# Optimization experiments

Measured on AMD Instinct MI355X. Metric: run time of the kernel, lower is better.

Reference implementation:

```python
import jax, jax.numpy as jnp
import numpy as np

N = 50000          # nodes
E = 800000         # edges (avg degree 16)
C = 64             # hidden_channels
MC = 128           # message_channels = 2*C
EDGE_IN = 3 * C + 4
UPD_IN = C + MC + C


def _mlp(x, w1, b1, w2, b2, w3, b3):
    h1 = jax.nn.gelu(x @ w1 + b1, approximate=False)  # torch nn.GELU default = exact erf
    h2 = jax.nn.gelu(h1 @ w2 + b2, approximate=False)
    return h2 @ w3 + b3


def _layernorm(x, g, b, eps=1e-5):
    mu = x.mean(-1, keepdims=True)
    var = ((x - mu) ** 2).mean(-1, keepdims=True)
    return (x - mu) * jax.lax.rsqrt(var + eps) * g + b


def _forward(edge_index, coords, h, flow_dir, ln_g, ln_b,
             ew1, eb1, ew2, eb2, ew3, eb3,
             gw1, gb1, gw2, gb2,
             glw1, glb1, glw2, glb2, glw3, glb3,
             uw1, ub1, uw2, ub2, uw3, ub3, res_scale):
    x = coords[0]                       # [N,3]
    feat = _layernorm(h[0], ln_g, ln_b) # [N,C]
    u = flow_dir[0]
    u = u / (jnp.linalg.norm(u) + 1e-8)
    row, col = edge_index[0], edge_index[1]
    xi, xj = x[row], x[col]             # [E,3] gathers
    rel = xi - xj
    dist2 = (rel * rel).sum(-1, keepdims=True)
    xi_dot_u = (xi * u).sum(-1, keepdims=True)
    xj_dot_u = (xj * u).sum(-1, keepdims=True)
    rel_dot_u = (rel * u).sum(-1, keepdims=True)
    fi, fj = feat[row], feat[col]       # [E,C]
    fd = fi - fj
    edge_input = jnp.concatenate([fi, fj, fd, dist2, xi_dot_u, xj_dot_u, rel_dot_u], axis=-1)  # [E, 3C+4]
    edge_hidden = _mlp(edge_input, ew1, eb1, ew2, eb2, ew3, eb3)  # [E, MC]
    gate = jax.nn.sigmoid(jax.nn.gelu(edge_hidden @ gw1 + gb1, approximate=False) @ gw2 + gb2)  # [E,1]
    msg = gate * edge_hidden
    agg = jax.ops.segment_sum(msg, row, num_segments=N)                       # [N, MC]
    deg = jax.ops.segment_sum(jnp.ones((E, 1), feat.dtype), row, num_segments=N)
    agg = agg / jnp.maximum(deg, 1.0)
    global_feat = feat.mean(0, keepdims=True)                                  # [1,C]
    global_ctx = _mlp(global_feat, glw1, glb1, glw2, glb2, glw3, glb3)        # [1,C]
    global_node = jnp.broadcast_to(global_ctx, (feat.shape[0], global_ctx.shape[-1]))
    update_input = jnp.concatenate([feat, agg, global_node], axis=-1)          # [N, C+MC+C]
    dh = _mlp(update_input, uw1, ub1, uw2, ub2, uw3, ub3)                      # [N,C]
    return (jnp.tanh(res_scale) * dh)[None]                                    # [1,N,C]


def setup_inputs() -> dict:
    key = jax.random.key(0)
    ks = iter(jax.random.split(key, 40))
    def nrm(shape, scale=0.05):
        return (jax.random.normal(next(ks), shape, jnp.float32) * scale)
    return {
        "coords": jax.random.normal(next(ks), (1, N, 3), jnp.float32),
        "h": jax.random.normal(next(ks), (1, N, C), jnp.float32),
        "flow_dir": jax.random.normal(next(ks), (1, 3), jnp.float32),
        "edge_index": jax.random.randint(next(ks), (2, E), 0, N, dtype=jnp.int32),
        "ln_g": jnp.ones((C,), jnp.float32), "ln_b": jnp.zeros((C,), jnp.float32),
        "ew1": nrm((EDGE_IN, MC)), "eb1": jnp.zeros((MC,), jnp.float32),
        "ew2": nrm((MC, MC)), "eb2": jnp.zeros((MC,), jnp.float32),
        "ew3": nrm((MC, MC)), "eb3": jnp.zeros((MC,), jnp.float32),
        "gw1": nrm((MC, MC)), "gb1": jnp.zeros((MC,), jnp.float32),
        "gw2": nrm((MC, 1)), "gb2": jnp.zeros((1,), jnp.float32),
        "glw1": nrm((C, C)), "glb1": jnp.zeros((C,), jnp.float32),
        "glw2": nrm((C, C)), "glb2": jnp.zeros((C,), jnp.float32),
        "glw3": nrm((C, C)), "glb3": jnp.zeros((C,), jnp.float32),
        "uw1": nrm((UPD_IN, MC)), "ub1": jnp.zeros((MC,), jnp.float32),
        "uw2": nrm((MC, MC)), "ub2": jnp.zeros((MC,), jnp.float32),
        "uw3": nrm((MC, C)), "ub3": jnp.zeros((C,), jnp.float32),
        "res_scale": jnp.float32(0.15),
    }


def reference(coords, h, flow_dir, edge_index, ln_g, ln_b,
              ew1, eb1, ew2, eb2, ew3, eb3,
              gw1, gb1, gw2, gb2,
              glw1, glb1, glw2, glb2, glw3, glb3,
              uw1, ub1, uw2, ub2, uw3, ub3, res_scale):
    return _forward(edge_index, coords, h, flow_dir, ln_g, ln_b,
                    ew1, eb1, ew2, eb2, ew3, eb3,
                    gw1, gb1, gw2, gb2,
                    glw1, glb1, glw2, glb2, glw3, glb3,
                    uw1, ub1, uw2, ub2, uw3, ub3, res_scale)
```

## Files before the change

kernel.cpp:

```cpp
#include <hip/hip_runtime.h>
#include <hip/hip_bf16.h>
#include <math.h>

#define N_NODES 50000
#define N_EDGES 800000
#define CDIM 64
#define MCDIM 128
#define GSUM_REP 32

#define XS1 168
#define HS  136
#define UST 264

typedef __attribute__((ext_vector_type(8))) short short8;
typedef __attribute__((ext_vector_type(4))) float floatx4;
typedef __attribute__((ext_vector_type(2))) float f32x2;

__device__ __forceinline__ float gelu_fast(float x) {
    float z = fabsf(x) * 0.70710678f;
    float w = fmaf(z, fmaf(z, fmaf(z, fmaf(z, 0.078108f, 0.000972f),
                                   0.230389f), 0.278393f), 1.0f);
    float w2 = w * w;
    float r = __builtin_amdgcn_rcpf(w2 * w2);
    float m = 0.5f * fabsf(x);
    return fmaf(-m, r, fmaf(0.5f, x, m));
}

__device__ __forceinline__ f32x2 gelu_pk(f32x2 x) {
    f32x2 ax = __builtin_elementwise_abs(x);
    f32x2 z = ax * 0.70710678f;
    f32x2 w = z * (z * (z * (z * 0.078108f + 0.000972f) + 0.230389f)
                   + 0.278393f) + 1.0f;
    f32x2 w2 = w * w;
    f32x2 w4 = w2 * w2;
    f32x2 r;
    r.x = __builtin_amdgcn_rcpf(w4.x);
    r.y = __builtin_amdgcn_rcpf(w4.y);
    f32x2 m = 0.5f * ax;
    return 0.5f * x + m - m * r;
}

__device__ __forceinline__ unsigned short f2bf(float f) {
    unsigned int u = __float_as_uint(f);
    unsigned int r = u + 0x7fffu + ((u >> 16) & 1u);
    return (unsigned short)(r >> 16);
}
__device__ __forceinline__ float bf2f(unsigned int lo16) {
    return __uint_as_float(lo16 << 16);
}
__device__ __forceinline__ unsigned int f2bf2(float lo, float hi) {
    __hip_bfloat162 v = __float22bfloat162_rn(make_float2(lo, hi));
    union { __hip_bfloat162 b; unsigned int u; } cv;
    cv.b = v;
    return cv.u;
}
__device__ __forceinline__ ushort4 pack4(float4 v) {
    ushort4 r;
    r.x = f2bf(v.x); r.y = f2bf(v.y); r.z = f2bf(v.z); r.w = f2bf(v.w);
    return r;
}

#define F1_OFF 0
#define F2_OFF (5 * 4096)
#define F3_OFF (9 * 4096)
#define FG_OFF (13 * 4096)
#define FU1_OFF (17 * 4096)
#define FU2_OFF (25 * 4096)
#define FU3_OFF (29 * 4096)
#define FRAG_TOTAL (29 * 4096 + 4 * 2048)

__global__ __launch_bounds__(256) void prep_frags(
    const float* __restrict__ ew1, const float* __restrict__ ew2,
    const float* __restrict__ ew3, const float* __restrict__ gw1,
    const float* __restrict__ eb3, const float* __restrict__ gb1,
    const float* __restrict__ uw1, const float* __restrict__ uw2,
    const float* __restrict__ uw3, unsigned short* __restrict__ frags,
    int* __restrict__ deg_int, float* __restrict__ gsum,
    float* __restrict__ egb) {
    int idx = blockIdx.x * 256 + threadIdx.x;
    if (idx < N_NODES) deg_int[idx] = 0;
    if (idx < GSUM_REP * 64) gsum[idx] = 0.0f;
    if (idx < 128) {
        float s = gb1[idx];
        for (int jj = 0; jj < 128; jj++) s += eb3[jj] * gw1[jj * 128 + idx];
        egb[idx] = s;
    }
    if (idx >= FRAG_TOTAL) return;
    if (idx < F2_OFF) {
        int chunk = idx >> 12;
        int rem = idx & 4095;
        int ct = rem >> 9;
        int lane = (rem >> 3) & 63;
        int j = rem & 7;
        int k = chunk * 32 + (lane >> 4) * 8 + j;
        int n = ct * 16 + (lane & 15);
        float v;
        if (k < 64)       v = ew1[k * 128 + n] + ew1[(128 + k) * 128 + n];
        else if (k < 128) v = ew1[k * 128 + n] - ew1[(64 + k) * 128 + n];
        else if (k < 132) v = ew1[(192 + k - 128) * 128 + n];
        else              v = 0.0f;
        frags[idx] = f2bf(v);
    } else if (idx >= FG_OFF && idx < FU1_OFF) {
        int chunk = idx >> 12;
        int rem = idx & 4095;
        int ct = rem >> 9;
        int lane = (rem >> 3) & 63;
        int j = rem & 7;
        int k = (chunk - 13) * 32 + (lane >> 4) * 8 + j;
        int n = ct * 16 + (lane & 15);
        float s = 0.0f;
        for (int jj = 0; jj < 128; jj++) s += ew3[k * 128 + jj] * gw1[jj * 128 + n];
        frags[idx] = f2bf(s);
    } else if (idx < FU3_OFF) {
        int chunk = idx >> 12;
        int rem = idx & 4095;
        int ct = rem >> 9;
        int lane = (rem >> 3) & 63;
        int j = rem & 7;
        const float* W; int kbase;
        if (chunk < 9)       { W = ew2; kbase = (chunk - 5) * 32; }
        else if (chunk < 13) { W = ew3; kbase = (chunk - 9) * 32; }
        else if (chunk < 25) { W = uw1; kbase = (chunk - 17) * 32; }
        else                 { W = uw2; kbase = (chunk - 25) * 32; }
        int k = kbase + (lane >> 4) * 8 + j;
        int n = ct * 16 + (lane & 15);
        frags[idx] = f2bf(W[k * 128 + n]);
    } else {
        int rem = idx - FU3_OFF;
        int chunk = rem >> 11;
        int r = rem & 2047;
        int ct = r >> 9;
        int lane = (r >> 3) & 63;
        int j = r & 7;
        int k = chunk * 32 + (lane >> 4) * 8 + j;
        int n = ct * 16 + (lane & 15);
        frags[idx] = f2bf(uw3[k * 64 + n]);
    }
}

template <int NCT>
__device__ __forceinline__ void bias_init(floatx4* acc,
                                          const float* __restrict__ bias, int lane) {
    int c = lane & 15;
#pragma unroll
    for (int ct = 0; ct < NCT; ct++) {
        float b = bias[ct * 16 + c];
        acc[ct][0] = b; acc[ct][1] = b; acc[ct][2] = b; acc[ct][3] = b;
    }
}

template <int NCH, int NCT>
__device__ __forceinline__ void mfma_layer(const unsigned short* Xl, int xs,
                                           const unsigned short* __restrict__ F,
                                           int lane, floatx4* acc) {
    int q = lane >> 4, c = lane & 15;
    const unsigned short* xrow = Xl + c * xs + q * 8;
    for (int k0 = 0; k0 < NCH; k0++) {
        short8 a = *(const short8*)(xrow + k0 * 32);
#pragma unroll
        for (int ct = 0; ct < NCT; ct++) {
            short8 b = *(const short8*)(F + ((k0 * NCT + ct) * 64 + lane) * 8);
            acc[ct] = __builtin_amdgcn_mfma_f32_16x16x32_bf16(a, b, acc[ct], 0, 0, 0);
        }
    }
}

template <bool GELU, int NCT>
__device__ __forceinline__ void epilogue_store(floatx4* acc,
                                               unsigned short* dst, int xs, int lane) {
    int q = lane >> 4, c = lane & 15;
    unsigned short* base = dst + (q * 4) * xs + c;
#pragma unroll
    for (int ct = 0; ct < NCT; ct++) {
        f32x2 v01 = {acc[ct][0], acc[ct][1]};
        f32x2 v23 = {acc[ct][2], acc[ct][3]};
        if (GELU) { v01 = gelu_pk(v01); v23 = gelu_pk(v23); }
        unsigned int p01 = f2bf2(v01.x, v01.y), p23 = f2bf2(v23.x, v23.y);
        unsigned short* p = base + ct * 16;
        p[0]      = (unsigned short)p01;
        p[xs]     = (unsigned short)(p01 >> 16);
        p[2 * xs] = (unsigned short)p23;
        p[3 * xs] = (unsigned short)(p23 >> 16);
    }
}

__global__ __launch_bounds__(256) void ln_count_kernel(
    const float* __restrict__ h, const float* __restrict__ ln_g,
    const float* __restrict__ ln_b, const float* __restrict__ flow_dir,
    const int* __restrict__ eidx, unsigned short* __restrict__ featb,
    float* __restrict__ gsum, float* __restrict__ u_out,
    int* __restrict__ deg_int) {
    int t = threadIdx.x;
    int ln = t >> 6;
    int c = t & 63;
    int n = blockIdx.x * 4 + ln;

    float x = h[n * CDIM + c];
    float s = x;
#pragma unroll
    for (int off = 32; off > 0; off >>= 1) s += __shfl_xor(s, off, 64);
    float mu = s * (1.0f / 64.0f);
    float d = x - mu;
    float v = d * d;
#pragma unroll
    for (int off = 32; off > 0; off >>= 1) v += __shfl_xor(v, off, 64);
    float rs = 1.0f / sqrtf(v * (1.0f / 64.0f) + 1e-5f);
    float f = d * rs * ln_g[c] + ln_b[c];
    featb[n * CDIM + c] = f2bf(f);

    __shared__ float fs[4][64];
    fs[ln][c] = f;
    __syncthreads();
    if (t < 64) {
        float p = fs[0][t] + fs[1][t] + fs[2][t] + fs[3][t];
        atomicAdd(&gsum[(blockIdx.x & (GSUM_REP - 1)) * 64 + t], p);
        int e = blockIdx.x * 64 + t;
        atomicAdd(&deg_int[eidx[e]], 1);
    }
    if (blockIdx.x == 0 && t == 0) {
        float ux = flow_dir[0], uy = flow_dir[1], uz = flow_dir[2];
        float nrm = sqrtf(ux * ux + uy * uy + uz * uz) + 1e-8f;
        u_out[0] = ux / nrm;
        u_out[1] = uy / nrm;
        u_out[2] = uz / nrm;
    }
}

__global__ __launch_bounds__(1024) void mid_kernel(
    const int* __restrict__ deg_int, int* __restrict__ rowstart,
    int* __restrict__ cursor,
    const float* __restrict__ gsum,
    const float* __restrict__ glw1, const float* __restrict__ glb1,
    const float* __restrict__ glw2, const float* __restrict__ glb2,
    const float* __restrict__ glw3, const float* __restrict__ glb3,
    const float* __restrict__ res_scale,
    unsigned short* __restrict__ gctxb, float* __restrict__ tres) {
    int t = threadIdx.x;
    if (blockIdx.x == 0) {
        __shared__ int wsum[16];
        __shared__ int run;
        int wid = t >> 6, lane = t & 63;
        int4 vs[13];
#pragma unroll
        for (int chunk = 0; chunk < 13; chunk++) {
            int base = chunk * 4096 + t * 4;
            int4 v = {0, 0, 0, 0};
            if (base + 3 < N_NODES) {
                v = *(const int4*)(deg_int + base);
            } else {
                if (base < N_NODES) v.x = deg_int[base];
                if (base + 1 < N_NODES) v.y = deg_int[base + 1];
                if (base + 2 < N_NODES) v.z = deg_int[base + 2];
                if (base + 3 < N_NODES) v.w = deg_int[base + 3];
            }
            vs[chunk] = v;
        }
        if (t == 0) run = 0;
        __syncthreads();
#pragma unroll
        for (int chunk = 0; chunk < 13; chunk++) {
            int base = chunk * 4096 + t * 4;
            int4 v = vs[chunk];
            int s1 = v.x, s2 = s1 + v.y, s3 = s2 + v.z, s4 = s3 + v.w;
            int x = s4;
#pragma unroll
            for (int off = 1; off < 64; off <<= 1) {
                int y = __shfl_up(x, off, 64);
                if (lane >= off) x += y;
            }
            if (lane == 63) wsum[wid] = x;
            __syncthreads();
            if (t < 16) {
                int sv = wsum[t];
#pragma unroll
                for (int off = 1; off < 16; off <<= 1) {
                    int y = __shfl_up(sv, off, 16);
                    if (t >= off) sv += y;
                }
                wsum[t] = sv;
            }
            __syncthreads();
            int run_l = run;
            int wpre = (wid == 0) ? 0 : wsum[wid - 1];
            int toff = run_l + wpre + (x - s4);
            int e0 = toff, e1 = toff + s1, e2 = toff + s2, e3 = toff + s3;
            if (base <= N_NODES) rowstart[base] = e0;
            if (base + 1 <= N_NODES) rowstart[base + 1] = e1;
            if (base + 2 <= N_NODES) rowstart[base + 2] = e2;
            if (base + 3 <= N_NODES) rowstart[base + 3] = e3;
            if (base < N_NODES) cursor[base] = e0;
            if (base + 1 < N_NODES) cursor[base + 1] = e1;
            if (base + 2 < N_NODES) cursor[base + 2] = e2;
            if (base + 3 < N_NODES) cursor[base + 3] = e3;
            __syncthreads();
            if (t == 0) run = run_l + wsum[15];
            __syncthreads();
        }
    } else {
        __shared__ float a[64], b[64];
        float s = 0.0f;
        if (t < 64) {
            float acc = 0.0f;
            for (int r = 0; r < GSUM_REP; r++) acc += gsum[r * 64 + t];
            a[t] = acc * (1.0f / (float)N_NODES);
        }
        __syncthreads();
        if (t < 64) {
            s = glb1[t];
            for (int k = 0; k < 64; k++) s += a[k] * glw1[k * 64 + t];
            b[t] = gelu_fast(s);
        }
        __syncthreads();
        if (t < 64) {
            s = glb2[t];
            for (int k = 0; k < 64; k++) s += b[k] * glw2[k * 64 + t];
        }
        __syncthreads();
        if (t < 64) a[t] = gelu_fast(s);
        __syncthreads();
        if (t < 64) {
            s = glb3[t];
            for (int k = 0; k < 64; k++) s += a[k] * glw3[k * 64 + t];
            gctxb[t] = f2bf(s);
        }
        if (t == 0) *tres = tanhf(res_scale[0]);
    }
}

struct SmemE {
    unsigned short x1[64 * XS1];
    float gate[64];
    int pos[64];
    int rows[64];
};

__global__ __launch_bounds__(256, 5) void edge_kernel(
    const float* __restrict__ coords, const int* __restrict__ eidx,
    const unsigned short* __restrict__ featb, const float* __restrict__ u,
    const unsigned short* __restrict__ frags,
    const float* __restrict__ eb1, const float* __restrict__ eb2,
    const float* __restrict__ eb3,
    const float* __restrict__ egb, const float* __restrict__ gw2,
    const float* __restrict__ gb2,
    int* __restrict__ cursor, unsigned short* __restrict__ msg,
    float* __restrict__ agg, int use_msg) {
    __shared__ SmemE sm;
    int t = threadIdx.x;
    int wv = t >> 6;
    int lane = t & 63;
    int e0 = blockIdx.x * 64;
    unsigned short* slice = sm.x1 + wv * 16 * XS1;

    {
        int le = t >> 2, sub = t & 3;
        int e = e0 + le;
        int row = eidx[e];
        int col = eidx[N_EDGES + e];
        const uint4* fi4 = (const uint4*)(featb + (long)row * CDIM);
        const uint4* fj4 = (const uint4*)(featb + (long)col * CDIM);
        unsigned short* xr = sm.x1 + le * XS1;
        *(uint4*)(xr + sub * 16) = fi4[sub * 2];
        *(uint4*)(xr + sub * 16 + 8) = fi4[sub * 2 + 1];
        *(uint4*)(xr + 64 + sub * 16) = fj4[sub * 2];
        *(uint4*)(xr + 64 + sub * 16 + 8) = fj4[sub * 2 + 1];
        ushort4 z = {0, 0, 0, 0};
        if (sub == 0) {
            sm.rows[le] = row;
            sm.pos[le] = atomicAdd(&cursor[row], 1);
            float xix = coords[row * 3], xiy = coords[row * 3 + 1], xiz = coords[row * 3 + 2];
            float xjx = coords[col * 3], xjy = coords[col * 3 + 1], xjz = coords[col * 3 + 2];
            float rx = xix - xjx, ry = xiy - xjy, rz = xiz - xjz;
            float ux = u[0], uy = u[1], uz = u[2];
            float4 sc;
            sc.x = rx * rx + ry * ry + rz * rz;
            sc.y = xix * ux + xiy * uy + xiz * uz;
            sc.z = xjx * ux + xjy * uy + xjz * uz;
            sc.w = rx * ux + ry * uy + rz * uz;
            *(ushort4*)(xr + 128) = pack4(sc);
        } else if (sub == 1) {
            *(ushort4*)(xr + 132) = z; *(ushort4*)(xr + 136) = z; *(ushort4*)(xr + 140) = z;
        } else if (sub == 2) {
            *(ushort4*)(xr + 144) = z; *(ushort4*)(xr + 148) = z;
        } else {
            *(ushort4*)(xr + 152) = z; *(ushort4*)(xr + 156) = z;
        }
    }
    __syncthreads();

    floatx4 acc[8];

    bias_init<8>(acc, eb1, lane);
    mfma_layer<5, 8>(slice, XS1, frags + F1_OFF, lane, acc);
    epilogue_store<true, 8>(acc, slice, HS, lane);
    __syncthreads();

    bias_init<8>(acc, eb2, lane);
    mfma_layer<4, 8>(slice, HS, frags + F2_OFF, lane, acc);
    epilogue_store<true, 8>(acc, slice, HS, lane);
    __syncthreads();

    bias_init<8>(acc, egb, lane);
    mfma_layer<4, 8>(slice, HS, frags + FG_OFF, lane, acc);
    {
        int q = lane >> 4, c = lane & 15;
        f32x2 p01 = {0.0f, 0.0f}, p23 = {0.0f, 0.0f};
#pragma unroll
        for (int ct = 0; ct < 8; ct++) {
            float w2 = gw2[ct * 16 + c];
            f32x2 g01 = gelu_pk((f32x2){acc[ct][0], acc[ct][1]});
            f32x2 g23 = gelu_pk((f32x2){acc[ct][2], acc[ct][3]});
            p01 += g01 * w2;
            p23 += g23 * w2;
        }
        float p[4] = {p01.x, p01.y, p23.x, p23.y};
#pragma unroll
        for (int i = 0; i < 4; i++) {
#pragma unroll
            for (int mask = 1; mask < 16; mask <<= 1) p[i] += __shfl_xor(p[i], mask, 64);
        }
        if (c == 0) {
            float gb = gb2[0];
#pragma unroll
            for (int i = 0; i < 4; i++) {
                float z = p[i] + gb;
                sm.gate[wv * 16 + q * 4 + i] = 1.0f / (1.0f + __expf(-z));
            }
        }
    }

    floatx4 h3[8];
    bias_init<8>(h3, eb3, lane);
    mfma_layer<4, 8>(slice, HS, frags + F3_OFF, lane, h3);

    if (use_msg) {
        {
            int q = lane >> 4, c = lane & 15;
            unsigned short* base = slice + (q * 4) * HS + c;
            float gv[4];
#pragma unroll
            for (int i = 0; i < 4; i++) gv[i] = sm.gate[wv * 16 + q * 4 + i];
#pragma unroll
            for (int ct = 0; ct < 8; ct++) {
                unsigned int p01 = f2bf2(h3[ct][0] * gv[0], h3[ct][1] * gv[1]);
                unsigned int p23 = f2bf2(h3[ct][2] * gv[2], h3[ct][3] * gv[3]);
                unsigned short* p = base + ct * 16;
                p[0] = (unsigned short)p01;
                p[HS] = (unsigned short)(p01 >> 16);
                p[2 * HS] = (unsigned short)p23;
                p[3 * HS] = (unsigned short)(p23 >> 16);
            }
        }
        __syncthreads();
        {
            int le = t >> 2, sub = t & 3;
            long base = (long)sm.pos[le] * MCDIM;
            const unsigned short* src = sm.x1 + (le >> 4) * 16 * XS1 + (le & 15) * HS;
#pragma unroll
            for (int m = 0; m < 4; m++) {
                int off = m * 32 + sub * 8;
                *(short8*)(msg + base + off) = *(const short8*)(src + off);
            }
        }
    } else {
        int q = lane >> 4, c = lane & 15;
#pragma unroll
        for (int i = 0; i < 4; i++) {
            int e = wv * 16 + q * 4 + i;
            int row = sm.rows[e];
            float g = sm.gate[e];
            float* agr = agg + (long)row * MCDIM;
#pragma unroll
            for (int ct = 0; ct < 8; ct++)
                atomicAdd(agr + ct * 16 + c, g * h3[ct][i]);
        }
    }
}

__global__ __launch_bounds__(256) void gather_kernel(
    const int* __restrict__ rowstart, const unsigned short* __restrict__ msg,
    const float* __restrict__ agg, int use_msg,
    unsigned short* __restrict__ aggb) {
    int wv = threadIdx.x >> 6, lane = threadIdx.x & 63;
    int n = blockIdx.x * 4 + wv;
    if (n >= N_NODES) return;
    int rs = rowstart[n], re = rowstart[n + 1];
    int deg = re - rs;
    float a0 = 0.0f, a1 = 0.0f, a2 = 0.0f, a3 = 0.0f;
    if (use_msg) {
        const unsigned short* base = msg + (long)rs * MCDIM;
        int pairs = deg >> 1;
        for (int i = 0; i < pairs; i++) {
            uint2 v = *(const uint2*)(base + i * 256 + lane * 4);
            a0 += bf2f(v.x & 0xffffu); a1 += bf2f(v.x >> 16);
            a2 += bf2f(v.y & 0xffffu); a3 += bf2f(v.y >> 16);
        }
        if ((deg & 1) && lane < 32) {
            uint2 v = *(const uint2*)(base + (deg - 1) * MCDIM + lane * 4);
            a0 += bf2f(v.x & 0xffffu); a1 += bf2f(v.x >> 16);
            a2 += bf2f(v.y & 0xffffu); a3 += bf2f(v.y >> 16);
        }
        a0 += __shfl_xor(a0, 32, 64);
        a1 += __shfl_xor(a1, 32, 64);
        a2 += __shfl_xor(a2, 32, 64);
        a3 += __shfl_xor(a3, 32, 64);
    } else if (lane < 32) {
        const float4 v = *(const float4*)(agg + (long)n * MCDIM + lane * 4);
        a0 = v.x; a1 = v.y; a2 = v.z; a3 = v.w;
    }
    if (lane < 32) {
        float inv = 1.0f / fmaxf((float)deg, 1.0f);
        uint2 o;
        o.x = f2bf2(a0 * inv, a1 * inv);
        o.y = f2bf2(a2 * inv, a3 * inv);
        *(uint2*)(aggb + (long)n * MCDIM + lane * 4) = o;
    }
}

struct SmemU {
    unsigned short ui[64 * UST];
};

__global__ __launch_bounds__(256, 4) void update_kernel(
    const unsigned short* __restrict__ featb, const unsigned short* __restrict__ aggb,
    const unsigned short* __restrict__ gctxb, const float* __restrict__ tres,
    const unsigned short* __restrict__ frags,
    const float* __restrict__ ub1, const float* __restrict__ ub2,
    const float* __restrict__ ub3,
    float* __restrict__ out) {
    __shared__ SmemU sm;
    int t = threadIdx.x;
    int wv = t >> 6;
    int lane = t & 63;
    int n0 = blockIdx.x * 64;
    unsigned short* slice = sm.ui + wv * 16 * UST;

    {
        int ln = t >> 2, sub = t & 3;
        int n = n0 + ln;
        unsigned short* ur = sm.ui + ln * UST;
        if (n < N_NODES) {
            const uint4* f4 = (const uint4*)(featb + (long)n * CDIM);
            *(uint4*)(ur + sub * 16) = f4[sub * 2];
            *(uint4*)(ur + sub * 16 + 8) = f4[sub * 2 + 1];
            const uint4* a4 = (const uint4*)(aggb + (long)n * MCDIM);
            *(uint4*)(ur + 64 + sub * 32) = a4[sub * 4];
            *(uint4*)(ur + 64 + sub * 32 + 8) = a4[sub * 4 + 1];
            *(uint4*)(ur + 64 + sub * 32 + 16) = a4[sub * 4 + 2];
            *(uint4*)(ur + 64 + sub * 32 + 24) = a4[sub * 4 + 3];
            const uint4* g4 = (const uint4*)gctxb;
            *(uint4*)(ur + 192 + sub * 16) = g4[sub * 2];
            *(uint4*)(ur + 192 + sub * 16 + 8) = g4[sub * 2 + 1];
        } else {
            uint4 z = {0, 0, 0, 0};
#pragma unroll
            for (int m = 0; m < 8; m++) *(uint4*)(ur + sub * 64 + m * 8) = z;
        }
    }
    __syncthreads();

    floatx4 acc[8];
    bias_init<8>(acc, ub1, lane);
    mfma_layer<8, 8>(slice, UST, frags + FU1_OFF, lane, acc);
    epilogue_store<true, 8>(acc, slice, HS, lane);
    __syncthreads();

    bias_init<8>(acc, ub2, lane);
    mfma_layer<4, 8>(slice, HS, frags + FU2_OFF, lane, acc);
    epilogue_store<true, 8>(acc, slice, HS, lane);
    __syncthreads();

    floatx4 acc3[4];
    bias_init<4>(acc3, ub3, lane);
    mfma_layer<4, 4>(slice, HS, frags + FU3_OFF, lane, acc3);
    {
        int q = lane >> 4, c = lane & 15;
        float tr = *tres;
#pragma unroll
        for (int ct = 0; ct < 4; ct++) {
#pragma unroll
            for (int i = 0; i < 4; i++) {
                int n = n0 + wv * 16 + q * 4 + i;
                if (n < N_NODES) out[(long)n * CDIM + ct * 16 + c] = acc3[ct][i] * tr;
            }
        }
    }
}

extern "C" void kernel_launch(void* const* d_in, const int* in_sizes, int n_in,
                              void* d_out, int out_size, void* d_ws, size_t ws_size,
                              hipStream_t stream) {
    const float* coords = (const float*)d_in[0];
    const float* h = (const float*)d_in[1];
    const float* flow = (const float*)d_in[2];
    const int* eidx = (const int*)d_in[3];
    const float* ln_g = (const float*)d_in[4];
    const float* ln_b = (const float*)d_in[5];
    const float* ew1 = (const float*)d_in[6];
    const float* eb1 = (const float*)d_in[7];
    const float* ew2 = (const float*)d_in[8];
    const float* eb2 = (const float*)d_in[9];
    const float* ew3 = (const float*)d_in[10];
    const float* eb3 = (const float*)d_in[11];
    const float* gw1 = (const float*)d_in[12];
    const float* gb1 = (const float*)d_in[13];
    const float* gw2 = (const float*)d_in[14];
    const float* gb2 = (const float*)d_in[15];
    const float* glw1 = (const float*)d_in[16];
    const float* glb1 = (const float*)d_in[17];
    const float* glw2 = (const float*)d_in[18];
    const float* glb2 = (const float*)d_in[19];
    const float* glw3 = (const float*)d_in[20];
    const float* glb3 = (const float*)d_in[21];
    const float* uw1 = (const float*)d_in[22];
    const float* ub1 = (const float*)d_in[23];
    const float* uw2 = (const float*)d_in[24];
    const float* ub2 = (const float*)d_in[25];
    const float* uw3 = (const float*)d_in[26];
    const float* ub3 = (const float*)d_in[27];
    const float* res = (const float*)d_in[28];

    char* base = (char*)d_ws;
    unsigned short* frags = (unsigned short*)base;
    unsigned short* featb = (unsigned short*)(base + FRAG_TOTAL * 2);
    unsigned short* aggb = featb + (size_t)N_NODES * CDIM;
    unsigned short* gctxb = aggb + (size_t)N_NODES * MCDIM;
    float* gsum = (float*)(gctxb + 64);
    float* u = gsum + GSUM_REP * 64;
    float* tres = u + 4;
    float* egb = tres + 1;
    int* rowstart = (int*)(egb + 128);
    int* cursor = rowstart + (N_NODES + 1);
    int* deg_int = cursor + N_NODES;
    char* tail = (char*)(deg_int + N_NODES);
    tail = (char*)(((uintptr_t)tail + 255) & ~(uintptr_t)255);
    size_t head_bytes = (size_t)(tail - base);
    size_t msg_bytes = (size_t)N_EDGES * MCDIM * 2;
    int use_msg = (ws_size >= head_bytes + msg_bytes) ? 1 : 0;
    unsigned short* msg = (unsigned short*)tail;
    float* agg = (float*)tail;

    if (!use_msg)
        hipMemsetAsync(agg, 0, (size_t)N_NODES * MCDIM * sizeof(float), stream);

    prep_frags<<<FRAG_TOTAL / 256, 256, 0, stream>>>(ew1, ew2, ew3, gw1,
                                                     eb3, gb1,
                                                     uw1, uw2, uw3, frags,
                                                     deg_int, gsum, egb);
    ln_count_kernel<<<N_NODES / 4, 256, 0, stream>>>(h, ln_g, ln_b, flow, eidx,
                                                     featb, gsum, u, deg_int);
    mid_kernel<<<2, 1024, 0, stream>>>(deg_int, rowstart, cursor, gsum,
                                       glw1, glb1, glw2, glb2, glw3, glb3,
                                       res, gctxb, tres);
    edge_kernel<<<N_EDGES / 64, 256, 0, stream>>>(coords, eidx, featb, u, frags,
                                                  eb1, eb2, eb3, egb, gw2, gb2,
                                                  cursor, msg, agg, use_msg);
    gather_kernel<<<(N_NODES + 3) / 4, 256, 0, stream>>>(rowstart, msg, agg,
                                                         use_msg, aggb);
    update_kernel<<<(N_NODES + 63) / 64, 256, 0, stream>>>(featb, aggb, gctxb,
                                                           tres, frags,
                                                           ub1, ub2, ub3,
                                                           (float*)d_out);
}
```

Measured before the change: 497.9 us.

## Process two 16-edge tiles per wave in edge MLP to reuse weight fragments

The edge kernel now runs 2 waves per block instead of 4, and each wave computes two 16-row MFMA tiles at once. Each weight fragment loaded from global/L2 is therefore reused for two MFMAs, halving weight-fragment traffic per edge. The gate value is now kept in registers, which removes its shared-memory array and a round trip. In exchange, register pressure doubles, since each wave holds two accumulator sets, and occupancy falls (launch bounds 128 threads, 3 blocks per CU), which may reduce latency hiding for the gathers.

Result: slower. 663.3 us (+33.2%).

```diff
diff --git a/kernel.cpp b/kernel.cpp
--- a/kernel.cpp
+++ b/kernel.cpp
@@ -165,6 +165,26 @@
     }
 }
 
+template <int NCH, int NCT>
+__device__ __forceinline__ void mfma_layer2(const unsigned short* XlA,
+                                            const unsigned short* XlB, int xs,
+                                            const unsigned short* __restrict__ F,
+                                            int lane, floatx4* accA, floatx4* accB) {
+    int q = lane >> 4, c = lane & 15;
+    const unsigned short* xrowA = XlA + c * xs + q * 8;
+    const unsigned short* xrowB = XlB + c * xs + q * 8;
+    for (int k0 = 0; k0 < NCH; k0++) {
+        short8 aA = *(const short8*)(xrowA + k0 * 32);
+        short8 aB = *(const short8*)(xrowB + k0 * 32);
+#pragma unroll
+        for (int ct = 0; ct < NCT; ct++) {
+            short8 b = *(const short8*)(F + ((k0 * NCT + ct) * 64 + lane) * 8);
+            accA[ct] = __builtin_amdgcn_mfma_f32_16x16x32_bf16(aA, b, accA[ct], 0, 0, 0);
+            accB[ct] = __builtin_amdgcn_mfma_f32_16x16x32_bf16(aB, b, accB[ct], 0, 0, 0);
+        }
+    }
+}
+
 template <bool GELU, int NCT>
 __device__ __forceinline__ void epilogue_store(floatx4* acc,
                                                unsigned short* dst, int xs, int lane) {
@@ -181,6 +201,44 @@
         p[xs]     = (unsigned short)(p01 >> 16);
         p[2 * xs] = (unsigned short)p23;
         p[3 * xs] = (unsigned short)(p23 >> 16);
+    }
+}
+
+__device__ __forceinline__ void gate_reduce(const floatx4* acc,
+                                            const float* __restrict__ gw2,
+                                            float gb, int lane, float* gv) {
+    int c = lane & 15;
+    f32x2 p01 = {0.0f, 0.0f}, p23 = {0.0f, 0.0f};
+#pragma unroll
+    for (int ct = 0; ct < 8; ct++) {
+        float w2 = gw2[ct * 16 + c];
+        f32x2 g01 = gelu_pk((f32x2){acc[ct][0], acc[ct][1]});
+        f32x2 g23 = gelu_pk((f32x2){acc[ct][2], acc[ct][3]});
+        p01 += g01 * w2;
+        p23 += g23 * w2;
+    }
+    float p[4] = {p01.x, p01.y, p23.x, p23.y};
+#pragma unroll
+    for (int i = 0; i < 4; i++) {
+#pragma unroll
+        for (int mask = 1; mask < 16; mask <<= 1) p[i] += __shfl_xor(p[i], mask, 64);
+        gv[i] = 1.0f / (1.0f + __expf(-(p[i] + gb)));
+    }
+}
+
+__device__ __forceinline__ void scaled_store(const floatx4* h3, const float* gv,
+                                             unsigned short* dst, int lane) {
+    int q = lane >> 4, c = lane & 15;
+    unsigned short* bp = dst + (q * 4) * HS + c;
+#pragma unroll
+    for (int ct = 0; ct < 8; ct++) {
+        unsigned int p01 = f2bf2(h3[ct][0] * gv[0], h3[ct][1] * gv[1]);
+        unsigned int p23 = f2bf2(h3[ct][2] * gv[2], h3[ct][3] * gv[3]);
+        unsigned short* p = bp + ct * 16;
+        p[0] = (unsigned short)p01;
+        p[HS] = (unsigned short)(p01 >> 16);
+        p[2 * HS] = (unsigned short)p23;
+        p[3 * HS] = (unsigned short)(p23 >> 16);
     }
 }
 
@@ -329,12 +387,11 @@
 
 struct SmemE {
     unsigned short x1[64 * XS1];
-    float gate[64];
     int pos[64];
     int rows[64];
 };
 
-__global__ __launch_bounds__(256, 5) void edge_kernel(
+__global__ __launch_bounds__(128, 3) void edge_kernel(
     const float* __restrict__ coords, const int* __restrict__ eidx,
     const unsigned short* __restrict__ featb, const float* __restrict__ u,
     const unsigned short* __restrict__ frags,
@@ -349,24 +406,26 @@
     int wv = t >> 6;
     int lane = t & 63;
     int e0 = blockIdx.x * 64;
-    unsigned short* slice = sm.x1 + wv * 16 * XS1;
+    unsigned short* slice = sm.x1 + wv * 32 * XS1;
 
     {
-        int le = t >> 2, sub = t & 3;
-        int e = e0 + le;
+        int le = lane >> 1, sub = lane & 1;
+        int ew = wv * 32 + le;
+        int e = e0 + ew;
         int row = eidx[e];
         int col = eidx[N_EDGES + e];
         const uint4* fi4 = (const uint4*)(featb + (long)row * CDIM);
         const uint4* fj4 = (const uint4*)(featb + (long)col * CDIM);
-        unsigned short* xr = sm.x1 + le * XS1;
-        *(uint4*)(xr + sub * 16) = fi4[sub * 2];
-        *(uint4*)(xr + sub * 16 + 8) = fi4[sub * 2 + 1];
-        *(uint4*)(xr + 64 + sub * 16) = fj4[sub * 2];
-        *(uint4*)(xr + 64 + sub * 16 + 8) = fj4[sub * 2 + 1];
+        unsigned short* xr = slice + le * XS1;
+#pragma unroll
+        for (int m = 0; m < 4; m++) {
+            *(uint4*)(xr + sub * 32 + m * 8) = fi4[sub * 4 + m];
+            *(uint4*)(xr + 64 + sub * 32 + m * 8) = fj4[sub * 4 + m];
+        }
         ushort4 z = {0, 0, 0, 0};
         if (sub == 0) {
-            sm.rows[le] = row;
-            sm.pos[le] = atomicAdd(&cursor[row], 1);
+            sm.rows[ew] = row;
+            sm.pos[ew] = atomicAdd(&cursor[row], 1);
             float xix = coords[row * 3], xiy = coords[row * 3 + 1], xiz = coords[row * 3 + 2];
             float xjx = coords[col * 3], xjy = coords[col * 3 + 1], xjz = coords[col * 3 + 2];
             float rx = xix - xjx, ry = xiy - xjy, rz = xiz - xjz;
@@ -377,87 +436,57 @@
             sc.z = xjx * ux + xjy * uy + xjz * uz;
             sc.w = rx * ux + ry * uy + rz * uz;
             *(ushort4*)(xr + 128) = pack4(sc);
-        } else if (sub == 1) {
             *(ushort4*)(xr + 132) = z; *(ushort4*)(xr + 136) = z; *(ushort4*)(xr + 140) = z;
-        } else if (sub == 2) {
+        } else {
             *(ushort4*)(xr + 144) = z; *(ushort4*)(xr + 148) = z;
-        } else {
             *(ushort4*)(xr + 152) = z; *(ushort4*)(xr + 156) = z;
         }
     }
     __syncthreads();
 
-    floatx4 acc[8];
-
-    bias_init<8>(acc, eb1, lane);
-    mfma_layer<5, 8>(slice, XS1, frags + F1_OFF, lane, acc);
-    epilogue_store<true, 8>(acc, slice, HS, lane);
+    floatx4 accA[8], accB[8];
+
+    bias_init<8>(accA, eb1, lane);
+#pragma unroll
+    for (int ct = 0; ct < 8; ct++) accB[ct] = accA[ct];
+    mfma_layer2<5, 8>(slice, slice + 16 * XS1, XS1, frags + F1_OFF, lane, accA, accB);
+    epilogue_store<true, 8>(accA, slice, HS, lane);
+    epilogue_store<true, 8>(accB, slice + 16 * HS, HS, lane);
     __syncthreads();
 
-    bias_init<8>(acc, eb2, lane);
-    mfma_layer<4, 8>(slice, HS, frags + F2_OFF, lane, acc);
-    epilogue_store<true, 8>(acc, slice, HS, lane);
+    bias_init<8>(accA, eb2, lane);
+#pragma unroll
+    for (int ct = 0; ct < 8; ct++) accB[ct] = accA[ct];
+    mfma_layer2<4, 8>(slice, slice + 16 * HS, HS, frags + F2_OFF, lane, accA, accB);
+    epilogue_store<true, 8>(accA, slice, HS, lane);
+    epilogue_store<true, 8>(accB, slice + 16 * HS, HS, lane);
     __syncthreads();
 
-    bias_init<8>(acc, egb, lane);
-    mfma_layer<4, 8>(slice, HS, frags + FG_OFF, lane, acc);
-    {
-        int q = lane >> 4, c = lane & 15;
-        f32x2 p01 = {0.0f, 0.0f}, p23 = {0.0f, 0.0f};
-#pragma unroll
-        for (int ct = 0; ct < 8; ct++) {
-            float w2 = gw2[ct * 16 + c];
-            f32x2 g01 = gelu_pk((f32x2){acc[ct][0], acc[ct][1]});
-            f32x2 g23 = gelu_pk((f32x2){acc[ct][2], acc[ct][3]});
-            p01 += g01 * w2;
-            p23 += g23 * w2;
-        }
-        float p[4] = {p01.x, p01.y, p23.x, p23.y};
-#pragma unroll
-        for (int i = 0; i < 4; i++) {
-#pragma unroll
-            for (int mask = 1; mask < 16; mask <<= 1) p[i] += __shfl_xor(p[i], mask, 64);
-        }
-        if (c == 0) {
-            float gb = gb2[0];
-#pragma unroll
-            for (int i = 0; i < 4; i++) {
-                float z = p[i] + gb;
-                sm.gate[wv * 16 + q * 4 + i] = 1.0f / (1.0f + __expf(-z));
-            }
-        }
-    }
-
-    floatx4 h3[8];
-    bias_init<8>(h3, eb3, lane);
-    mfma_layer<4, 8>(slice, HS, frags + F3_OFF, lane, h3);
+    bias_init<8>(accA, egb, lane);
+#pragma unroll
+    for (int ct = 0; ct < 8; ct++) accB[ct] = accA[ct];
+    mfma_layer2<4, 8>(slice, slice + 16 * HS, HS, frags + FG_OFF, lane, accA, accB);
+    float gb = gb2[0];
+    float gvA[4], gvB[4];
+    gate_reduce(accA, gw2, gb, lane, gvA);
+    gate_reduce(accB, gw2, gb, lane, gvB);
+
+    bias_init<8>(accA, eb3, lane);
+#pragma unroll
+    for (int ct = 0; ct < 8; ct++) accB[ct] = accA[ct];
+    mfma_layer2<4, 8>(slice, slice + 16 * HS, HS, frags + F3_OFF, lane, accA, accB);
 
     if (use_msg) {
-        {
-            int q = lane >> 4, c = lane & 15;
-            unsigned short* base = slice + (q * 4) * HS + c;
-            float gv[4];
-#pragma unroll
-            for (int i = 0; i < 4; i++) gv[i] = sm.gate[wv * 16 + q * 4 + i];
-#pragma unroll
-            for (int ct = 0; ct < 8; ct++) {
-                unsigned int p01 = f2bf2(h3[ct][0] * gv[0], h3[ct][1] * gv[1]);
-                unsigned int p23 = f2bf2(h3[ct][2] * gv[2], h3[ct][3] * gv[3]);
-                unsigned short* p = base + ct * 16;
-                p[0] = (unsigned short)p01;
-                p[HS] = (unsigned short)(p01 >> 16);
-                p[2 * HS] = (unsigned short)p23;
-                p[3 * HS] = (unsigned short)(p23 >> 16);
-            }
-        }
+        scaled_store(accA, gvA, slice, lane);
+        scaled_store(accB, gvB, slice + 16 * HS, lane);
         __syncthreads();
         {
-            int le = t >> 2, sub = t & 3;
-            long base = (long)sm.pos[le] * MCDIM;
-            const unsigned short* src = sm.x1 + (le >> 4) * 16 * XS1 + (le & 15) * HS;
-#pragma unroll
-            for (int m = 0; m < 4; m++) {
-                int off = m * 32 + sub * 8;
+            int le = lane >> 1, sub = lane & 1;
+            long base = (long)sm.pos[wv * 32 + le] * MCDIM;
+            const unsigned short* src = slice + le * HS;
+#pragma unroll
+            for (int m = 0; m < 8; m++) {
+                int off = m * 16 + sub * 8;
                 *(short8*)(msg + base + off) = *(const short8*)(src + off);
             }
         }
@@ -465,13 +494,15 @@
         int q = lane >> 4, c = lane & 15;
 #pragma unroll
         for (int i = 0; i < 4; i++) {
-            int e = wv * 16 + q * 4 + i;
-            int row = sm.rows[e];
-            float g = sm.gate[e];
-            float* agr = agg + (long)row * MCDIM;
-#pragma unroll
-            for (int ct = 0; ct < 8; ct++)
-                atomicAdd(agr + ct * 16 + c, g * h3[ct][i]);
+            int rA = sm.rows[wv * 32 + q * 4 + i];
+            int rB = sm.rows[wv * 32 + 16 + q * 4 + i];
+            float* agrA = agg + (long)rA * MCDIM;
+            float* agrB = agg + (long)rB * MCDIM;
+#pragma unroll
+            for (int ct = 0; ct < 8; ct++) {
+                atomicAdd(agrA + ct * 16 + c, gvA[i] * accA[ct][i]);
+                atomicAdd(agrB + ct * 16 + c, gvB[i] * accB[ct][i]);
+            }
         }
     }
 }
@@ -651,7 +682,7 @@
     mid_kernel<<<2, 1024, 0, stream>>>(deg_int, rowstart, cursor, gsum,
                                        glw1, glb1, glw2, glb2, glw3, glb3,
                                        res, gctxb, tres);
-    edge_kernel<<<N_EDGES / 64, 256, 0, stream>>>(coords, eidx, featb, u, frags,
+    edge_kernel<<<N_EDGES / 64, 128, 0, stream>>>(coords, eidx, featb, u, frags,
                                                   eb1, eb2, eb3, egb, gw2, gb2,
                                                   cursor, msg, agg, use_msg);
     gather_kernel<<<(N_NODES + 3) / 4, 256, 0, stream>>>(rowstart, msg, agg,
```

## Split edge MLP across waves by output columns instead of edge rows

Applied to the files above, without the earlier changes.

The edge kernel's MFMA layers now assign each wave 32 output columns across all 64 edges, instead of 16 edges across all 128 columns. Each weight fragment is then loaded once per wave and reused across four row tiles, which cuts global/L2 weight-fragment traffic by about four times. The price is extra block-wide barriers between layers, since every wave now reads the full shared activation tile. The gate logit is now a partial sum per wave and is reduced through shared memory.

New measurement: 465.8 us. 6.5% less time.

```diff
diff --git a/kernel.cpp b/kernel.cpp
--- a/kernel.cpp
+++ b/kernel.cpp
@@ -165,6 +165,58 @@
     }
 }
 
+template <int NCH>
+__device__ __forceinline__ void mfma_nsplit(const unsigned short* x1, int rstride,
+                                            const unsigned short* __restrict__ F,
+                                            int lane, int w2,
+                                            floatx4 acc[4][2]) {
+    int q = lane >> 4, c = lane & 15;
+    for (int k0 = 0; k0 < NCH; k0++) {
+        short8 b0 = *(const short8*)(F + (((k0 * 8 + w2) * 64) + lane) * 8);
+        short8 b1 = *(const short8*)(F + (((k0 * 8 + w2 + 1) * 64) + lane) * 8);
+#pragma unroll
+        for (int rt = 0; rt < 4; rt++) {
+            short8 a = *(const short8*)(x1 + rt * (16 * XS1) + c * rstride
+                                        + q * 8 + k0 * 32);
+            acc[rt][0] = __builtin_amdgcn_mfma_f32_16x16x32_bf16(a, b0, acc[rt][0], 0, 0, 0);
+            acc[rt][1] = __builtin_amdgcn_mfma_f32_16x16x32_bf16(a, b1, acc[rt][1], 0, 0, 0);
+        }
+    }
+}
+
+__device__ __forceinline__ void bias_init2(floatx4 acc[4][2],
+                                           const float* __restrict__ bias,
+                                           int lane, int w) {
+    int c = lane & 15;
+    float b0 = bias[w * 32 + c], b1 = bias[w * 32 + 16 + c];
+#pragma unroll
+    for (int rt = 0; rt < 4; rt++) {
+        acc[rt][0][0] = b0; acc[rt][0][1] = b0; acc[rt][0][2] = b0; acc[rt][0][3] = b0;
+        acc[rt][1][0] = b1; acc[rt][1][1] = b1; acc[rt][1][2] = b1; acc[rt][1][3] = b1;
+    }
+}
+
+__device__ __forceinline__ void epi2_store(floatx4 acc[4][2],
+                                           unsigned short* x1, int lane, int w) {
+    int q = lane >> 4, c = lane & 15;
+#pragma unroll
+    for (int rt = 0; rt < 4; rt++) {
+        unsigned short* base = x1 + rt * (16 * XS1) + (q * 4) * HS + w * 32 + c;
+#pragma unroll
+        for (int ctl = 0; ctl < 2; ctl++) {
+            f32x2 v01 = {acc[rt][ctl][0], acc[rt][ctl][1]};
+            f32x2 v23 = {acc[rt][ctl][2], acc[rt][ctl][3]};
+            v01 = gelu_pk(v01); v23 = gelu_pk(v23);
+            unsigned int p01 = f2bf2(v01.x, v01.y), p23 = f2bf2(v23.x, v23.y);
+            unsigned short* p = base + ctl * 16;
+            p[0]      = (unsigned short)p01;
+            p[HS]     = (unsigned short)(p01 >> 16);
+            p[2 * HS] = (unsigned short)p23;
+            p[3 * HS] = (unsigned short)(p23 >> 16);
+        }
+    }
+}
+
 template <bool GELU, int NCT>
 __device__ __forceinline__ void epilogue_store(floatx4* acc,
                                                unsigned short* dst, int xs, int lane) {
@@ -329,7 +381,7 @@
 
 struct SmemE {
     unsigned short x1[64 * XS1];
-    float gate[64];
+    float gatep[4][64];
     int pos[64];
     int rows[64];
 };
@@ -349,7 +401,8 @@
     int wv = t >> 6;
     int lane = t & 63;
     int e0 = blockIdx.x * 64;
-    unsigned short* slice = sm.x1 + wv * 16 * XS1;
+    int q = lane >> 4, c = lane & 15;
+    int w2 = wv * 2;
 
     {
         int le = t >> 2, sub = t & 3;
@@ -387,67 +440,86 @@
     }
     __syncthreads();
 
-    floatx4 acc[8];
-
-    bias_init<8>(acc, eb1, lane);
-    mfma_layer<5, 8>(slice, XS1, frags + F1_OFF, lane, acc);
-    epilogue_store<true, 8>(acc, slice, HS, lane);
-    __syncthreads();
-
-    bias_init<8>(acc, eb2, lane);
-    mfma_layer<4, 8>(slice, HS, frags + F2_OFF, lane, acc);
-    epilogue_store<true, 8>(acc, slice, HS, lane);
-    __syncthreads();
-
-    bias_init<8>(acc, egb, lane);
-    mfma_layer<4, 8>(slice, HS, frags + FG_OFF, lane, acc);
+    floatx4 acc[4][2];
+
+    bias_init2(acc, eb1, lane, wv);
+    mfma_nsplit<5>(sm.x1, XS1, frags + F1_OFF, lane, w2, acc);
+    __syncthreads();
+    epi2_store(acc, sm.x1, lane, wv);
+    __syncthreads();
+
+    bias_init2(acc, eb2, lane, wv);
+    mfma_nsplit<4>(sm.x1, HS, frags + F2_OFF, lane, w2, acc);
+    __syncthreads();
+    epi2_store(acc, sm.x1, lane, wv);
+    __syncthreads();
+
+    bias_init2(acc, egb, lane, wv);
+    mfma_nsplit<4>(sm.x1, HS, frags + FG_OFF, lane, w2, acc);
     {
-        int q = lane >> 4, c = lane & 15;
-        f32x2 p01 = {0.0f, 0.0f}, p23 = {0.0f, 0.0f};
-#pragma unroll
-        for (int ct = 0; ct < 8; ct++) {
-            float w2 = gw2[ct * 16 + c];
-            f32x2 g01 = gelu_pk((f32x2){acc[ct][0], acc[ct][1]});
-            f32x2 g23 = gelu_pk((f32x2){acc[ct][2], acc[ct][3]});
-            p01 += g01 * w2;
-            p23 += g23 * w2;
-        }
-        float p[4] = {p01.x, p01.y, p23.x, p23.y};
+#pragma unroll
+        for (int rt = 0; rt < 4; rt++) {
+            float w2v0 = gw2[wv * 32 + c];
+            float w2v1 = gw2[wv * 32 + 16 + c];
+            f32x2 g01a = gelu_pk((f32x2){acc[rt][0][0], acc[rt][0][1]});
+            f32x2 g23a = gelu_pk((f32x2){acc[rt][0][2], acc[rt][0][3]});
+            f32x2 g01b = gelu_pk((f32x2){acc[rt][1][0], acc[rt][1][1]});
+            f32x2 g23b = gelu_pk((f32x2){acc[rt][1][2], acc[rt][1][3]});
+            float p[4];
+            p[0] = g01a.x * w2v0 + g01b.x * w2v1;
+            p[1] = g01a.y * w2v0 + g01b.y * w2v1;
+            p[2] = g23a.x * w2v0 + g23b.x * w2v1;
+            p[3] = g23a.y * w2v0 + g23b.y * w2v1;
+#pragma unroll
+            for (int i = 0; i < 4; i++) {
+#pragma unroll
+                for (int mask = 1; mask < 16; mask <<= 1)
+                    p[i] += __shfl_xor(p[i], mask, 64);
+            }
+            if (c == 0) {
+#pragma unroll
+                for (int i = 0; i < 4; i++)
+                    sm.gatep[wv][rt * 16 + q * 4 + i] = p[i];
+            }
+        }
+    }
+
+    floatx4 acch[4][2];
+    bias_init2(acch, eb3, lane, wv);
+    mfma_nsplit<4>(sm.x1, HS, frags + F3_OFF, lane, w2, acch);
+    __syncthreads();
+
+    float gb = gb2[0];
+    float g4[4][4];
+#pragma unroll
+    for (int rt = 0; rt < 4; rt++) {
 #pragma unroll
         for (int i = 0; i < 4; i++) {
-#pragma unroll
-            for (int mask = 1; mask < 16; mask <<= 1) p[i] += __shfl_xor(p[i], mask, 64);
-        }
-        if (c == 0) {
-            float gb = gb2[0];
-#pragma unroll
-            for (int i = 0; i < 4; i++) {
-                float z = p[i] + gb;
-                sm.gate[wv * 16 + q * 4 + i] = 1.0f / (1.0f + __expf(-z));
-            }
-        }
-    }
-
-    floatx4 h3[8];
-    bias_init<8>(h3, eb3, lane);
-    mfma_layer<4, 8>(slice, HS, frags + F3_OFF, lane, h3);
+            int e = rt * 16 + q * 4 + i;
+            float z = sm.gatep[0][e] + sm.gatep[1][e] + sm.gatep[2][e]
+                    + sm.gatep[3][e] + gb;
+            g4[rt][i] = 1.0f / (1.0f + __expf(-z));
+        }
+    }
 
     if (use_msg) {
         {
-            int q = lane >> 4, c = lane & 15;
-            unsigned short* base = slice + (q * 4) * HS + c;
-            float gv[4];
-#pragma unroll
-            for (int i = 0; i < 4; i++) gv[i] = sm.gate[wv * 16 + q * 4 + i];
-#pragma unroll
-            for (int ct = 0; ct < 8; ct++) {
-                unsigned int p01 = f2bf2(h3[ct][0] * gv[0], h3[ct][1] * gv[1]);
-                unsigned int p23 = f2bf2(h3[ct][2] * gv[2], h3[ct][3] * gv[3]);
-                unsigned short* p = base + ct * 16;
-                p[0] = (unsigned short)p01;
-                p[HS] = (unsigned short)(p01 >> 16);
-                p[2 * HS] = (unsigned short)p23;
-                p[3 * HS] = (unsigned short)(p23 >> 16);
+#pragma unroll
+            for (int rt = 0; rt < 4; rt++) {
+                unsigned short* base = sm.x1 + rt * (16 * XS1) + (q * 4) * HS
+                                     + wv * 32 + c;
+#pragma unroll
+                for (int ctl = 0; ctl < 2; ctl++) {
+                    unsigned int p01 = f2bf2(acch[rt][ctl][0] * g4[rt][0],
+                                             acch[rt][ctl][1] * g4[rt][1]);
+                    unsigned int p23 = f2bf2(acch[rt][ctl][2] * g4[rt][2],
+                                             acch[rt][ctl][3] * g4[rt][3]);
+                    unsigned short* p = base + ctl * 16;
+                    p[0]      = (unsigned short)p01;
+                    p[HS]     = (unsigned short)(p01 >> 16);
+                    p[2 * HS] = (unsigned short)p23;
+                    p[3 * HS] = (unsigned short)(p23 >> 16);
+                }
             }
         }
         __syncthreads();
@@ -462,16 +534,16 @@
             }
         }
     } else {
-        int q = lane >> 4, c = lane & 15;
-#pragma unroll
-        for (int i = 0; i < 4; i++) {
-            int e = wv * 16 + q * 4 + i;
-            int row = sm.rows[e];
-            float g = sm.gate[e];
-            float* agr = agg + (long)row * MCDIM;
-#pragma unroll
-            for (int ct = 0; ct < 8; ct++)
-                atomicAdd(agr + ct * 16 + c, g * h3[ct][i]);
+#pragma unroll
+        for (int rt = 0; rt < 4; rt++) {
+#pragma unroll
+            for (int i = 0; i < 4; i++) {
+                int row = sm.rows[rt * 16 + q * 4 + i];
+                float* agr = agg + (long)row * MCDIM + wv * 32 + c;
+#pragma unroll
+                for (int ctl = 0; ctl < 2; ctl++)
+                    atomicAdd(agr + ctl * 16, g4[rt][i] * acch[rt][ctl][i]);
+            }
         }
     }
 }
```
